# Kernel optimization log

Hardware: AMD Instinct MI355X
Metric: run time of the kernel (lower is better)

The kernel has to match this reference:

```python
import jax, jax.numpy as jnp
import numpy as np

IN_CH, OUT_CH, K, POOL = 3, 16, 3, 2

def setup_inputs() -> dict:
    key = jax.random.key(0)
    kx, kw, kb = jax.random.split(key, 3)
    B, H, W = 64, 512, 512
    x = jax.random.normal(kx, (B, IN_CH, H, W), dtype=jnp.float32)
    fan_in = IN_CH * K * K
    bound = 1.0 / np.sqrt(fan_in)
    weight = jax.random.uniform(kw, (OUT_CH, IN_CH, K, K), dtype=jnp.float32, minval=-bound, maxval=bound)
    bias = jax.random.uniform(kb, (OUT_CH,), dtype=jnp.float32, minval=-bound, maxval=bound)
    return {"x": x, "weight": weight, "bias": bias}

def reference(x, weight, bias):
    # Conv2d, stride 1, VALID padding (matches in_h - k + 1 in kernel)
    y = jax.lax.conv_general_dilated(
        x, weight, window_strides=(1, 1), padding="VALID",
        dimension_numbers=("NCHW", "OIHW", "NCHW"))
    y = y + bias[None, :, None, None]  # [B, OC, Hc, Wc]
    B, C, Hc, Wc = y.shape
    Hp, Wp = Hc // POOL, Wc // POOL
    # Average pool 2x2 (floor-cropped like the CUDA kernel's integer division)
    y = y[:, :, :Hp * POOL, :Wp * POOL].reshape(B, C, Hp, POOL, Wp, POOL).mean(axis=(3, 5))
    # Sigmoid then sum over channel + spatial dims -> one scalar per batch element
    return jax.nn.sigmoid(y).sum(axis=(1, 2, 3))
```

## Files before the change

kernel.cpp:

```cpp
#include <hip/hip_runtime.h>


#define IC 3
#define OCH 16
#define HH 512
#define WW 512
#define HP 255
#define SROWS 5
#define STRIPS 51

__device__ __forceinline__ float fast_sigmoid(float v) {
    float e = __expf(-v);
    return __builtin_amdgcn_rcpf(1.0f + e);
}

__global__ void build_weff(const float* __restrict__ w,
                           const float* __restrict__ bias,
                           float* __restrict__ ws)
{
    const int i = threadIdx.x;
    for (int idx = i; idx < IC * 4 * OCH * 4; idx += 256) {
        int kx = idx & 3;
        int oc = (idx >> 2) & 15;
        int icr = idx >> 6;
        int ic = icr >> 2;
        int ky = icr & 3;
        float s = 0.f;
#pragma unroll
        for (int py = 0; py < 2; ++py) {
            int r = ky - py;
            if (r < 0 || r > 2) continue;
#pragma unroll
            for (int px = 0; px < 2; ++px) {
                int c = kx - px;
                if (c < 0 || c > 2) continue;
                s += w[((oc * IC + ic) * 3 + r) * 3 + c];
            }
        }
        ws[idx] = 0.25f * s;
    }
    if (i < OCH) ws[IC * 4 * OCH * 4 + i] = bias[i];
}

__global__ __launch_bounds__(128)
void conv_pool_sig_sum(const float* __restrict__ x,
                       const float* __restrict__ wws,
                       float* __restrict__ out)
{
    const int tid = threadIdx.x;
    const bool v1 = (tid < 127);
    const int c0 = 4 * tid;
    const int b = blockIdx.y;
    const int hp0 = blockIdx.x * SROWS;
    const int tail = v1 ? 4 : 0;

    const float* xb = x + ((size_t)b * IC * HH + (size_t)2 * hp0) * WW + c0;
    const float* bp = wws + IC * 4 * OCH * 4;

    float lsA = 0.f, lsB = 0.f;

#pragma unroll 1
    for (int s = 0; s < SROWS; ++s) {
        float accA[OCH], accB[OCH];
#pragma unroll
        for (int oc = 0; oc < OCH; ++oc) { accA[oc] = bp[oc]; accB[oc] = bp[oc]; }

#pragma unroll
        for (int icr = 0; icr < IC * 4; ++icr) {
            const int ic = icr >> 2, r = icr & 3;
            const float* pr = xb + (size_t)ic * HH * WW + r * WW;
            const float4 a = *(const float4*)pr;
            const float2 t = *(const float2*)(pr + tail);
            const float* wp = wws + icr * 64;
#pragma unroll
            for (int oc = 0; oc < OCH; ++oc) {
                const float w0 = wp[4 * oc + 0], w1 = wp[4 * oc + 1];
                const float w2 = wp[4 * oc + 2], w3 = wp[4 * oc + 3];
                accA[oc] += a.x * w0 + a.y * w1 + a.z * w2 + a.w * w3;
                accB[oc] += a.z * w0 + a.w * w1 + t.x * w2 + t.y * w3;
            }
        }

#pragma unroll
        for (int oc = 0; oc < OCH; ++oc) {
            lsA += fast_sigmoid(accA[oc]);
            lsB += fast_sigmoid(accB[oc]);
        }
        xb += 2 * WW;
    }
    lsA += v1 ? lsB : 0.f;

#pragma unroll
    for (int off = 32; off > 0; off >>= 1)
        lsA += __shfl_xor(lsA, off, 64);
    if ((tid & 63) == 0) atomicAdd(out + b, lsA);
}

extern "C" void kernel_launch(void* const* d_in, const int* in_sizes, int n_in,
                              void* d_out, int out_size, void* d_ws, size_t ws_size,
                              hipStream_t stream) {
    const float* x = (const float*)d_in[0];
    const float* w = (const float*)d_in[1];
    const float* bias = (const float*)d_in[2];
    float* out = (float*)d_out;
    float* wws = (float*)d_ws;

    hipMemsetAsync(out, 0, out_size * sizeof(float), stream);
    build_weff<<<1, 256, 0, stream>>>(w, bias, wws);

    dim3 grid(STRIPS, 64);
    conv_pool_sig_sum<<<grid, 128, 0, stream>>>(x, wws, out);
}
```

Baseline: 391.2 us.

## Reuse overlapping input rows in registers and prefetch next rows mid-step

```diff
diff --git a/kernel.cpp b/kernel.cpp
--- a/kernel.cpp
+++ b/kernel.cpp
@@ -5,7 +5,6 @@
 #define OCH 16
 #define HH 512
 #define WW 512
-#define HP 255
 #define SROWS 5
 #define STRIPS 51
 
@@ -42,6 +41,64 @@
     if (i < OCH) ws[IC * 4 * OCH * 4 + i] = bias[i];
 }
 
+__device__ __forceinline__ void dot_row(const float4& a, const float2& t,
+                                        const float* __restrict__ wp,
+                                        float (&accA)[OCH], float (&accB)[OCH])
+{
+#pragma unroll
+    for (int oc = 0; oc < OCH; ++oc) {
+        const float w0 = wp[4 * oc + 0], w1 = wp[4 * oc + 1];
+        const float w2 = wp[4 * oc + 2], w3 = wp[4 * oc + 3];
+        accA[oc] = fmaf(a.x, w0, fmaf(a.y, w1, fmaf(a.z, w2, fmaf(a.w, w3, accA[oc]))));
+        accB[oc] = fmaf(a.z, w0, fmaf(a.w, w1, fmaf(t.x, w2, fmaf(t.y, w3, accB[oc]))));
+    }
+}
+
+template<int S0, int S1, int S2, int S3>
+__device__ __forceinline__ void srow_step(const float* __restrict__ xcb,
+                                          const float* __restrict__ wws,
+                                          const float (&bv)[OCH],
+                                          float4 (&A)[IC][4], float2 (&T)[IC][4],
+                                          int yf, int tail,
+                                          float& lsA, float& lsB)
+{
+    float accA[OCH], accB[OCH];
+#pragma unroll
+    for (int oc = 0; oc < OCH; ++oc) { accA[oc] = bv[oc]; accB[oc] = bv[oc]; }
+
+#pragma unroll
+    for (int ic = 0; ic < IC; ++ic) {
+        dot_row(A[ic][S0], T[ic][S0], wws + (ic * 4 + 0) * 64, accA, accB);
+        dot_row(A[ic][S1], T[ic][S1], wws + (ic * 4 + 1) * 64, accA, accB);
+    }
+
+    {
+        const int y0 = yf     > 511 ? 511 : yf;
+        const int y1 = yf + 1 > 511 ? 511 : yf + 1;
+#pragma unroll
+        for (int ic = 0; ic < IC; ++ic) {
+            const float* p0 = xcb + ((size_t)ic * HH + y0) * WW;
+            const float* p1 = xcb + ((size_t)ic * HH + y1) * WW;
+            A[ic][S0] = *(const float4*)p0;
+            T[ic][S0] = *(const float2*)(p0 + tail);
+            A[ic][S1] = *(const float4*)p1;
+            T[ic][S1] = *(const float2*)(p1 + tail);
+        }
+    }
+
+#pragma unroll
+    for (int ic = 0; ic < IC; ++ic) {
+        dot_row(A[ic][S2], T[ic][S2], wws + (ic * 4 + 2) * 64, accA, accB);
+        dot_row(A[ic][S3], T[ic][S3], wws + (ic * 4 + 3) * 64, accA, accB);
+    }
+
+#pragma unroll
+    for (int oc = 0; oc < OCH; ++oc) {
+        lsA += fast_sigmoid(accA[oc]);
+        lsB += fast_sigmoid(accB[oc]);
+    }
+}
+
 __global__ __launch_bounds__(128)
 void conv_pool_sig_sum(const float* __restrict__ x,
                        const float* __restrict__ wws,
@@ -54,40 +111,35 @@
     const int hp0 = blockIdx.x * SROWS;
     const int tail = v1 ? 4 : 0;
 
-    const float* xb = x + ((size_t)b * IC * HH + (size_t)2 * hp0) * WW + c0;
+    const float* xcb = x + (size_t)b * IC * HH * WW + c0;
     const float* bp = wws + IC * 4 * OCH * 4;
 
-    float lsA = 0.f, lsB = 0.f;
+    float bv[OCH];
+#pragma unroll
+    for (int oc = 0; oc < OCH; ++oc) bv[oc] = bp[oc];
 
-#pragma unroll 1
-    for (int s = 0; s < SROWS; ++s) {
-        float accA[OCH], accB[OCH];
+    float4 A[IC][4];
+    float2 T[IC][4];
+    const int y0 = 2 * hp0;
 #pragma unroll
-        for (int oc = 0; oc < OCH; ++oc) { accA[oc] = bp[oc]; accB[oc] = bp[oc]; }
-
+    for (int ic = 0; ic < IC; ++ic)
 #pragma unroll
-        for (int icr = 0; icr < IC * 4; ++icr) {
-            const int ic = icr >> 2, r = icr & 3;
-            const float* pr = xb + (size_t)ic * HH * WW + r * WW;
-            const float4 a = *(const float4*)pr;
-            const float2 t = *(const float2*)(pr + tail);
-            const float* wp = wws + icr * 64;
-#pragma unroll
-            for (int oc = 0; oc < OCH; ++oc) {
-                const float w0 = wp[4 * oc + 0], w1 = wp[4 * oc + 1];
-                const float w2 = wp[4 * oc + 2], w3 = wp[4 * oc + 3];
-                accA[oc] += a.x * w0 + a.y * w1 + a.z * w2 + a.w * w3;
-                accB[oc] += a.z * w0 + a.w * w1 + t.x * w2 + t.y * w3;
-            }
+        for (int r = 0; r < 4; ++r) {
+            const float* p = xcb + ((size_t)ic * HH + y0 + r) * WW;
+            A[ic][r] = *(const float4*)p;
+            T[ic][r] = *(const float2*)(p + tail);
         }
 
-#pragma unroll
-        for (int oc = 0; oc < OCH; ++oc) {
-            lsA += fast_sigmoid(accA[oc]);
-            lsB += fast_sigmoid(accB[oc]);
-        }
-        xb += 2 * WW;
+    float lsA = 0.f, lsB = 0.f;
+    int yn = y0 + 4;
+
+    srow_step<0, 1, 2, 3>(xcb, wws, bv, A, T, yn, tail, lsA, lsB); yn += 2;
+#pragma unroll 1
+    for (int k = 0; k < (SROWS - 1) / 2; ++k) {
+        srow_step<2, 3, 0, 1>(xcb, wws, bv, A, T, yn, tail, lsA, lsB); yn += 2;
+        srow_step<0, 1, 2, 3>(xcb, wws, bv, A, T, yn, tail, lsA, lsB); yn += 2;
     }
+
     lsA += v1 ? lsB : 0.f;
 
 #pragma unroll
```

Result: slower. 448.6 us (+14.7%).
